# Optimization experiments

Measured on AMD Instinct MI355X. Metric: run time of the kernel, lower is better.

The kernel has to match this reference:

```python
import jax, jax.numpy as jnp
import numpy as np

RES = 32
HEADS = 16
EMB = 1024
DIM_HEAD = EMB // HEADS
BATCH = 8
N = RES * RES
SCALE = DIM_HEAD ** -0.5


def _make_bias_idxs():
    # replicate the LeViT-style |dx|,|dy| offset indexing from __init__
    points = [(i, j) for i in range(RES) for j in range(RES)]
    offsets = {}
    idxs = []
    for p1 in points:
        for p2 in points:
            off = (abs(p1[0] - p2[0]), abs(p1[1] - p2[1]))
            if off not in offsets:
                offsets[off] = len(offsets)
            idxs.append(offsets[off])
    return np.asarray(idxs, dtype=np.int32).reshape(N, N), len(offsets)


def setup_inputs() -> dict:
    key = jax.random.key(0)
    k_x, k_qkv, k_b, k_o = jax.random.split(key, 4)
    bias_idxs, n_off = _make_bias_idxs()  # n_off == 1024 for a 32x32 grid
    return {
        "x": jax.random.normal(k_x, (BATCH, N, EMB), dtype=jnp.float32),
        "W_qkv": jax.random.normal(k_qkv, (3 * EMB, EMB), dtype=jnp.float32) * 0.02,
        "attention_biases": jax.random.normal(k_b, (HEADS, n_off), dtype=jnp.float32) * 0.02,
        "bias_idxs": jnp.asarray(bias_idxs),
        "W_out": jax.random.normal(k_o, (EMB, EMB), dtype=jnp.float32) * 0.02,
        "b_out": jnp.zeros((EMB,), dtype=jnp.float32),
    }


def reference(x, W_qkv, attention_biases, bias_idxs, W_out, b_out):
    B, n, E = x.shape
    # to_qkv: Linear(E, 3E, bias=False) -> x @ W^T
    qkv = x @ W_qkv.T  # [B, n, 3E]
    q, k, v = jnp.split(qkv, 3, axis=-1)

    def heads(t):  # b n (h d) -> b h n d
        return t.reshape(B, n, HEADS, DIM_HEAD).transpose(0, 2, 1, 3)

    q, k, v = heads(q), heads(k), heads(v)
    qk = jnp.einsum("bhnd,bhmd->bhnm", q, k) * SCALE  # [B, h, n, n]
    bias = attention_biases[:, bias_idxs]  # gather -> [h, n, n]
    qk = qk + bias[None]
    attn = jax.nn.softmax(qk, axis=-1)
    out = jnp.einsum("bhnm,bhmd->bhnd", attn, v)
    out = out.transpose(0, 2, 1, 3).reshape(B, n, E)  # b h n d -> b n (h d)
    # to_out: Linear(E, E) with bias (dropout p=0 is identity)
    return out @ W_out.T + b_out
```

## Files before the change

kernel.cpp:

```cpp
#include <hip/hip_runtime.h>

typedef __attribute__((ext_vector_type(8))) short bf16x8;
typedef __attribute__((ext_vector_type(4))) short bf16x4;
typedef __attribute__((ext_vector_type(4))) float f32x4;

#define L2E 1.44269504088896340736f
#define QSCL 0.18033688011112042f

__device__ inline unsigned short f2bf(float f) {
  union { float f; unsigned int u; } x; x.f = f;
  return (unsigned short)((x.u + 0x8000u) >> 16);
}
__device__ inline unsigned int f2bf2(float a, float b) {
  union { float f; unsigned int u; } xa, xb;
  xa.f = a; xb.f = b;
  return ((xa.u + 0x8000u) >> 16) | (((xb.u + 0x8000u) & 0xFFFF0000u));
}
__device__ inline unsigned int pk_bf16(float a, float b) {
#if __has_builtin(__builtin_amdgcn_cvt_pk_bf16_f32)
  typedef __attribute__((ext_vector_type(2))) __bf16 bfv2;
  union { bfv2 v; unsigned int u; } x;
  x.v = __builtin_amdgcn_cvt_pk_bf16_f32(a, b);
  return x.u;
#else
  return f2bf2(a, b);
#endif
}

__device__ inline void gl_lds16(const void* g, void* l) {
  __builtin_amdgcn_global_load_lds((const __attribute__((address_space(1))) void*)g,
                                   (__attribute__((address_space(3))) void*)l,
                                   16, 0, 0);
}

__device__ inline void vm_drain() {
  asm volatile("s_waitcnt vmcnt(0)" ::: "memory");
}
__device__ inline void vm_wait3() {
  asm volatile("s_waitcnt vmcnt(3)" ::: "memory");
}
__device__ inline void vm_wait8() {
  asm volatile("s_waitcnt vmcnt(8)" ::: "memory");
}

__device__ inline void wave_barrier() {
  asm volatile("" ::: "memory");
  __builtin_amdgcn_s_barrier();
  asm volatile("" ::: "memory");
}

#define N4_X  2097152
#define N4_WQ 786432
#define N4_WO 262144
__global__ void cast3_kernel(const float* __restrict__ x,
                             const float* __restrict__ wq,
                             const float* __restrict__ wo,
                             unsigned short* __restrict__ xb,
                             unsigned short* __restrict__ wqb,
                             unsigned short* __restrict__ wob) {
  int i = blockIdx.x * blockDim.x + threadIdx.x;
  int st = gridDim.x * blockDim.x;
  for (; i < N4_X + N4_WQ + N4_WO; i += st) {
    const float* src; unsigned short* dst; int j;
    if (i < N4_X)            { src = x;  dst = xb;  j = i; }
    else if (i < N4_X + N4_WQ){ src = wq; dst = wqb; j = i - N4_X; }
    else                     { src = wo; dst = wob; j = i - N4_X - N4_WQ; }
    float4 v = reinterpret_cast<const float4*>(src)[j];
    ushort4 o;
    o.x = f2bf(v.x); o.y = f2bf(v.y); o.z = f2bf(v.z); o.w = f2bf(v.w);
    reinterpret_cast<ushort4*>(dst)[j] = o;
  }
}

template <int MODE>
__device__ __forceinline__ void qkv_body(
    unsigned short* lds,
    const unsigned short* __restrict__ A,
    const unsigned short* __restrict__ Bm,
    unsigned short* __restrict__ qo,
    unsigned short* __restrict__ ko,
    unsigned short* __restrict__ vo,
    int tm, int tn) {
  const int tid = threadIdx.x;
  const int w = tid >> 6, lane = tid & 63;
  const int l15 = lane & 15, quad = lane >> 4;
  const int wmb = (w >> 2) * 128;
  const int wnb = (w & 3) * 64;
  const int rl = (w << 3) + (lane >> 3);
  const int scol = ((lane & 7) ^ ((lane >> 3) & 7)) << 3;
  const int rk = l15 & 7;

  const unsigned short* Ab = A + (size_t)(tm * 256) * 1024;
  const unsigned short* Bb = Bm + (size_t)(tn * 256) * 1024;

  unsigned short* sA0 = lds;
  unsigned short* sA1 = lds + 16384;
  unsigned short* sB0 = lds + 32768;
  unsigned short* sB1 = lds + 49152;

#define STG_HALF(Gb, R0, k0, Lb)                                              \
  do {                                                                        \
    gl_lds16((Gb) + (size_t)((R0) + rl) * 1024 + (k0) + scol,                 \
             (Lb) + ((R0) + (w << 3)) * 64);                                  \
    gl_lds16((Gb) + (size_t)((R0) + 64 + rl) * 1024 + (k0) + scol,            \
             (Lb) + ((R0) + 64 + (w << 3)) * 64);                             \
  } while (0)

#define LDF(buf, row, kk) \
  (*(const bf16x8*)&(buf)[(row) * 64 + ((((kk) * 4 + quad) ^ rk) << 3)])

  STG_HALF(Ab, 0, 0, sA0);  STG_HALF(Ab, 128, 0, sA0);
  STG_HALF(Bb, 0, 0, sB0);  STG_HALF(Bb, 128, 0, sB0);
  STG_HALF(Ab, 0, 64, sA1); STG_HALF(Ab, 128, 64, sA1);
  STG_HALF(Bb, 0, 64, sB1); STG_HALF(Bb, 128, 64, sB1);

  const f32x4 fz = {0.f, 0.f, 0.f, 0.f};
  f32x4 acc[8][4];
#pragma unroll
  for (int i = 0; i < 8; i++)
#pragma unroll
    for (int j = 0; j < 4; j++) acc[i][j] = fz;

  vm_wait8();
  wave_barrier();

  for (int t = 0; t < 16; ++t) {
    unsigned short* Ac = (t & 1) ? sA1 : sA0;
    unsigned short* Bc = (t & 1) ? sB1 : sB0;
    const int kf = (t + 2) << 6;
    bf16x8 a0[4][2], a1[4][2], b0[2][2], b1[2][2];

#pragma unroll
    for (int mt = 0; mt < 4; mt++)
#pragma unroll
      for (int kk = 0; kk < 2; kk++)
        a0[mt][kk] = LDF(Ac, wmb + mt * 16 + l15, kk);
#pragma unroll
    for (int nt = 0; nt < 2; nt++)
#pragma unroll
      for (int kk = 0; kk < 2; kk++)
        b0[nt][kk] = LDF(Bc, wnb + nt * 16 + l15, kk);
    wave_barrier();
    __builtin_amdgcn_s_setprio(1);
#pragma unroll
    for (int mt = 0; mt < 4; mt++)
#pragma unroll
      for (int nt = 0; nt < 2; nt++)
#pragma unroll
        for (int kk = 0; kk < 2; kk++)
          acc[mt][nt] = (MODE == 0)
            ? __builtin_amdgcn_mfma_f32_16x16x32_bf16(b0[nt][kk], a0[mt][kk], acc[mt][nt], 0, 0, 0)
            : __builtin_amdgcn_mfma_f32_16x16x32_bf16(a0[mt][kk], b0[nt][kk], acc[mt][nt], 0, 0, 0);
    __builtin_amdgcn_s_setprio(0);
    wave_barrier();

#pragma unroll
    for (int nt = 0; nt < 2; nt++)
#pragma unroll
      for (int kk = 0; kk < 2; kk++)
        b1[nt][kk] = LDF(Bc, wnb + (nt + 2) * 16 + l15, kk);
    wave_barrier();
    __builtin_amdgcn_s_setprio(1);
#pragma unroll
    for (int mt = 0; mt < 4; mt++)
#pragma unroll
      for (int nt = 0; nt < 2; nt++)
#pragma unroll
        for (int kk = 0; kk < 2; kk++)
          acc[mt][nt + 2] = (MODE == 0)
            ? __builtin_amdgcn_mfma_f32_16x16x32_bf16(b1[nt][kk], a0[mt][kk], acc[mt][nt + 2], 0, 0, 0)
            : __builtin_amdgcn_mfma_f32_16x16x32_bf16(a0[mt][kk], b1[nt][kk], acc[mt][nt + 2], 0, 0, 0);
    __builtin_amdgcn_s_setprio(0);
    wave_barrier();

#pragma unroll
    for (int mt = 0; mt < 4; mt++)
#pragma unroll
      for (int kk = 0; kk < 2; kk++)
        a1[mt][kk] = LDF(Ac, wmb + (mt + 4) * 16 + l15, kk);
    if (t < 14) { STG_HALF(Bb, 0, kf, Bc); STG_HALF(Bb, 128, kf, Bc); }
    wave_barrier();
    __builtin_amdgcn_s_setprio(1);
#pragma unroll
    for (int mt = 0; mt < 4; mt++)
#pragma unroll
      for (int nt = 0; nt < 2; nt++)
#pragma unroll
        for (int kk = 0; kk < 2; kk++)
          acc[mt + 4][nt] = (MODE == 0)
            ? __builtin_amdgcn_mfma_f32_16x16x32_bf16(b0[nt][kk], a1[mt][kk], acc[mt + 4][nt], 0, 0, 0)
            : __builtin_amdgcn_mfma_f32_16x16x32_bf16(a1[mt][kk], b0[nt][kk], acc[mt + 4][nt], 0, 0, 0);
    __builtin_amdgcn_s_setprio(0);
    wave_barrier();

    if (t < 14) { STG_HALF(Ab, 0, kf, Ac); STG_HALF(Ab, 128, kf, Ac); }
    wave_barrier();
    __builtin_amdgcn_s_setprio(1);
#pragma unroll
    for (int mt = 0; mt < 4; mt++)
#pragma unroll
      for (int nt = 0; nt < 2; nt++)
#pragma unroll
        for (int kk = 0; kk < 2; kk++)
          acc[mt + 4][nt + 2] = (MODE == 0)
            ? __builtin_amdgcn_mfma_f32_16x16x32_bf16(b1[nt][kk], a1[mt][kk], acc[mt + 4][nt + 2], 0, 0, 0)
            : __builtin_amdgcn_mfma_f32_16x16x32_bf16(a1[mt][kk], b1[nt][kk], acc[mt + 4][nt + 2], 0, 0, 0);
    __builtin_amdgcn_s_setprio(0);
    if (t < 14) vm_wait8();
    else if (t == 14) vm_drain();
    wave_barrier();
  }
#undef STG_HALF
#undef LDF

  const int bb = tm >> 2;
  const int n0 = (tm & 3) << 8;
  const int cb = (tn & 3) << 8;
  if (MODE == 0) {
    const float scl = (tn < 4) ? QSCL : 1.0f;
    unsigned short* dst = (tn < 4) ? qo : ko;
#pragma unroll
    for (int mt = 0; mt < 8; mt++) {
      int tok = n0 + wmb + mt * 16 + l15;
#pragma unroll
      for (int nt = 0; nt < 4; nt++) {
        int c = cb + wnb + nt * 16 + quad * 4;
        int hh = c >> 6, d0 = c & 63;
        uint2 val;
        val.x = f2bf2(acc[mt][nt][0] * scl, acc[mt][nt][1] * scl);
        val.y = f2bf2(acc[mt][nt][2] * scl, acc[mt][nt][3] * scl);
        *(uint2*)&dst[(((size_t)bb * 16 + hh) * 1024 + tok) * 64 + d0] = val;
      }
    }
  } else {
#pragma unroll
    for (int mt = 0; mt < 8; mt++) {
      int tok = n0 + wmb + mt * 16 + quad * 4;
#pragma unroll
      for (int nt = 0; nt < 4; nt++) {
        int c = cb + wnb + nt * 16 + l15;
        int hh = c >> 6, dd = c & 63;
        uint2 val;
        val.x = f2bf2(acc[mt][nt][0], acc[mt][nt][1]);
        val.y = f2bf2(acc[mt][nt][2], acc[mt][nt][3]);
        *(uint2*)&vo[(((size_t)bb * 16 + hh) * 64 + dd) * 1024 + tok] = val;
      }
    }
  }
}

__global__ __launch_bounds__(512, 2) void gemm_qkv(
    const unsigned short* __restrict__ A,
    const unsigned short* __restrict__ Bm,
    unsigned short* __restrict__ qo,
    unsigned short* __restrict__ ko,
    unsigned short* __restrict__ vo) {
  __shared__ unsigned short lds[65536];
  const int id = blockIdx.x;
  const int wg = (id & 7) * 48 + (id >> 3);
  const int tm = wg / 12, tn = wg - tm * 12;
  if (tn < 8) qkv_body<0>(lds, A, Bm, qo, ko, vo, tm, tn);
  else        qkv_body<1>(lds, A, Bm, qo, ko, vo, tm, tn);
}

__global__ __launch_bounds__(256, 2) void attn_kernel(
    const unsigned short* __restrict__ Q,
    const unsigned short* __restrict__ Kg,
    const unsigned short* __restrict__ Vt,
    const float* __restrict__ biases,
    unsigned short* __restrict__ Og) {
  __shared__ unsigned short sK[2][64 * 64];
  __shared__ unsigned short sV[2][64 * 64];
  __shared__ float sBias2[32 * 63];

  const int bx = blockIdx.x;
  const int bh = bx & 127, qt = bx >> 7;
  const int h = bh & 15, b = bh >> 4;
  const int tid = threadIdx.x, w = tid >> 6, lane = tid & 63;
  const int l15 = lane & 15, quad = lane >> 4;

  const size_t bhs = (size_t)(b * 16 + h);
  const unsigned short* qbase = Q + (bhs * 1024 + (size_t)qt * 256) * 64;
  const unsigned short* kbase = Kg + bhs * 1024 * 64;
  const unsigned short* vbase = Vt + bhs * 64 * 1024;

  for (int t = tid; t < 2048; t += 256) {
    int d = t >> 6, u = t & 63;
    if (u < 63) {
      int dj = u - 31; dj = dj < 0 ? -dj : dj;
      sBias2[d * 63 + u] = biases[h * 1024 + d * 32 + dj] * L2E;
    }
  }

  const int sr0 = w * 16 + (lane >> 3);
  const int sc8 = lane & 7;
  const int sw0 = sc8 ^ (lane >> 3);

  gl_lds16(kbase + (size_t)sr0 * 64 + sw0 * 8,        &sK[0][(w * 16) * 64]);
  gl_lds16(kbase + (size_t)(sr0 + 8) * 64 + sw0 * 8,  &sK[0][(w * 16 + 8) * 64]);
  gl_lds16(vbase + (size_t)sr0 * 1024 + sw0 * 8,      &sV[0][(w * 16) * 64]);
  gl_lds16(vbase + (size_t)(sr0 + 8) * 1024 + sw0 * 8,&sV[0][(w * 16 + 8) * 64]);

  bf16x8 qf[4][2];
#pragma unroll
  for (int qb = 0; qb < 4; qb++)
#pragma unroll
    for (int kd = 0; kd < 2; kd++)
      qf[qb][kd] = *(const bf16x8*)(qbase + (w * 64 + qb * 16 + l15) * 64 + kd * 32 + quad * 8);

  const int qg0 = qt * 256 + w * 64;
  const int qtw = __builtin_amdgcn_readfirstlane(qt * 8 + w * 2);
  int cc2[2][2];
#pragma unroll
  for (int qh = 0; qh < 2; qh++)
#pragma unroll
    for (int kp = 0; kp < 2; kp++)
      cc2[qh][kp] = qh * 16 + l15 - kp * 16 - quad * 4;

  const f32x4 fz = {0.f, 0.f, 0.f, 0.f};
  f32x4 of[4][4], osum[4];
#pragma unroll
  for (int i = 0; i < 4; i++) {
    osum[i] = fz;
#pragma unroll
    for (int j = 0; j < 4; j++) of[i][j] = fz;
  }
  const bf16x4 vones = {(short)0x3F80, (short)0x3F80, (short)0x3F80, (short)0x3F80};

  int buf = 0;
  for (int j0 = 0; j0 < 1024; j0 += 64) {
    vm_drain();
    __syncthreads();
    if (j0 + 64 < 1024) {
      int nb = buf ^ 1, jn = j0 + 64;
      gl_lds16(kbase + (size_t)(jn + sr0) * 64 + sw0 * 8,       &sK[nb][(w * 16) * 64]);
      gl_lds16(kbase + (size_t)(jn + sr0 + 8) * 64 + sw0 * 8,   &sK[nb][(w * 16 + 8) * 64]);
      gl_lds16(vbase + (size_t)sr0 * 1024 + jn + sw0 * 8,       &sV[nb][(w * 16) * 64]);
      gl_lds16(vbase + (size_t)(sr0 + 8) * 1024 + jn + sw0 * 8, &sV[nb][(w * 16 + 8) * 64]);
    }
    const unsigned short* K_ = sK[buf];
    const unsigned short* V_ = sV[buf];
    const int j5 = j0 >> 5;
    const int dh = qtw - j5;
    const float* b0 = sBias2 + abs(dh) * 63 + 31;
    const float* bM = sBias2 + abs(dh - 1) * 63 + 31;
    const float* bP = sBias2 + abs(dh + 1) * 63 + 31;

#pragma unroll
    for (int kvb = 0; kvb < 4; kvb++) {
      bf16x8 kf0 = *(const bf16x8*)&K_[(kvb * 16 + l15) * 64 + ((quad ^ (l15 & 7)) << 3)];
      bf16x8 kf1 = *(const bf16x8*)&K_[(kvb * 16 + l15) * 64 + (((4 + quad) ^ (l15 & 7)) << 3)];
      bf16x4 vf[4];
#pragma unroll
      for (int nt = 0; nt < 4; nt++) {
        int d = nt * 16 + l15;
        vf[nt] = *(const bf16x4*)&V_[d * 64 + (((kvb * 2 + (quad >> 1)) ^ (l15 & 7)) << 3) + (quad & 1) * 4];
      }
      const int kp = kvb & 1;
#pragma unroll
      for (int qb = 0; qb < 4; qb++) {
        f32x4 s4 = __builtin_amdgcn_mfma_f32_16x16x32_bf16(kf0, qf[qb][0], fz, 0, 0, 0);
        s4 = __builtin_amdgcn_mfma_f32_16x16x32_bf16(kf1, qf[qb][1], s4, 0, 0, 0);
        const float* bp = (qb < 2) ? ((kvb < 2) ? b0 : bM)
                                   : ((kvb < 2) ? bP : b0);
        const float* bq = bp + cc2[qb & 1][kp];
        float p0 = __builtin_amdgcn_exp2f(s4.x + bq[0]);
        float p1 = __builtin_amdgcn_exp2f(s4.y + bq[-1]);
        float p2 = __builtin_amdgcn_exp2f(s4.z + bq[-2]);
        float p3 = __builtin_amdgcn_exp2f(s4.w + bq[-3]);
        union { unsigned int u[2]; bf16x4 v; } pk;
        pk.u[0] = pk_bf16(p0, p1);
        pk.u[1] = pk_bf16(p2, p3);
#pragma unroll
        for (int nt = 0; nt < 4; nt++)
          of[qb][nt] = __builtin_amdgcn_mfma_f32_16x16x16bf16_1k(pk.v, vf[nt], of[qb][nt], 0, 0, 0);
        osum[qb] = __builtin_amdgcn_mfma_f32_16x16x16bf16_1k(pk.v, vones, osum[qb], 0, 0, 0);
      }
    }
    buf ^= 1;
  }

  const int kvq = quad * 4;
#pragma unroll
  for (int qb = 0; qb < 4; qb++)
#pragma unroll
    for (int r = 0; r < 4; r++) {
      float inv = __builtin_amdgcn_rcpf(osum[qb][r]);
      int n = qg0 + qb * 16 + kvq + r;
      size_t orow = ((size_t)b * 1024 + n) * 1024 + h * 64;
#pragma unroll
      for (int nt = 0; nt < 4; nt++)
        Og[orow + nt * 16 + l15] = f2bf(of[qb][nt][r] * inv);
    }
}

__global__ __launch_bounds__(256, 4) void gemm_out_k(
    const unsigned short* __restrict__ A,
    const unsigned short* __restrict__ Bm,
    const float* __restrict__ bias,
    float* __restrict__ out) {
  __shared__ unsigned short sA[3][128 * 32];
  __shared__ unsigned short sB[3][64 * 32];
  const int K = 1024;
  const int tid = threadIdx.x;
  const int w = tid >> 6, lane = tid & 63;
  const int l15 = lane & 15, quad = lane >> 4;
  const int tm = blockIdx.y, tn = blockIdx.x;

  const unsigned short* Ab = A + (size_t)(tm * 128) * K;
  const unsigned short* Bb = Bm + (size_t)(tn * 64) * K;

  const int srowA = w * 32 + (lane >> 2);
  const int srowB = w * 16 + (lane >> 2);
  const int scol = (((lane & 3) ^ ((lane >> 3) & 3))) * 8;
  const int rsw = (l15 >> 1) & 3;

  const f32x4 fz = {0.f, 0.f, 0.f, 0.f};
  f32x4 acc[2][4];
#pragma unroll
  for (int i = 0; i < 2; i++)
#pragma unroll
    for (int j = 0; j < 4; j++) acc[i][j] = fz;

#define OUT_STAGE(kn, nb)                                                          \
  do {                                                                             \
    gl_lds16(Ab + (size_t)srowA * K + (kn) + scol,        &sA[nb][(w * 32) * 32]);      \
    gl_lds16(Ab + (size_t)(srowA + 16) * K + (kn) + scol, &sA[nb][(w * 32 + 16) * 32]); \
    gl_lds16(Bb + (size_t)srowB * K + (kn) + scol,        &sB[nb][(w * 16) * 32]);      \
  } while (0)

  OUT_STAGE(0, 0);
  OUT_STAGE(32, 1);

  int bi = 0;
  for (int k0 = 0; k0 < K; k0 += 32) {
    if (k0 + 64 < K) vm_wait3(); else vm_drain();
    __syncthreads();
    if (k0 + 64 < K) {
      int nb = bi + 2; if (nb >= 3) nb -= 3;
      OUT_STAGE(k0 + 64, nb);
    }
    bf16x8 af[2], bfr[4];
#pragma unroll
    for (int mt = 0; mt < 2; mt++)
      af[mt] = *(const bf16x8*)&sA[bi][(w * 32 + mt * 16 + l15) * 32 + ((quad ^ rsw) << 3)];
#pragma unroll
    for (int nt = 0; nt < 4; nt++)
      bfr[nt] = *(const bf16x8*)&sB[bi][(nt * 16 + l15) * 32 + ((quad ^ rsw) << 3)];
#pragma unroll
    for (int mt = 0; mt < 2; mt++)
#pragma unroll
      for (int nt = 0; nt < 4; nt++)
        acc[mt][nt] = __builtin_amdgcn_mfma_f32_16x16x32_bf16(af[mt], bfr[nt], acc[mt][nt], 0, 0, 0);
    bi = bi + 1; if (bi == 3) bi = 0;
  }
#undef OUT_STAGE

  const int m0 = tm * 128 + w * 32, c0 = tn * 64;
#pragma unroll
  for (int mt = 0; mt < 2; mt++)
#pragma unroll
    for (int nt = 0; nt < 4; nt++)
#pragma unroll
      for (int r = 0; r < 4; r++) {
        int m = m0 + mt * 16 + quad * 4 + r;
        int c = c0 + nt * 16 + l15;
        out[(size_t)m * 1024 + c] = acc[mt][nt][r] + bias[c];
      }
}

extern "C" void kernel_launch(void* const* d_in, const int* in_sizes, int n_in,
                              void* d_out, int out_size, void* d_ws, size_t ws_size,
                              hipStream_t stream) {
  const float* x    = (const float*)d_in[0];
  const float* Wqkv = (const float*)d_in[1];
  const float* ab   = (const float*)d_in[2];
  const float* Wout = (const float*)d_in[4];
  const float* bout = (const float*)d_in[5];
  float* out = (float*)d_out;

  char* ws = (char*)d_ws;
  unsigned short* xb  = (unsigned short*)(ws);
  unsigned short* wqb = (unsigned short*)(ws + 16777216);
  unsigned short* wob = (unsigned short*)(ws + 23068672);
  unsigned short* qw  = (unsigned short*)(ws + 25165824);
  unsigned short* kw  = (unsigned short*)(ws + 41943040);
  unsigned short* vw  = (unsigned short*)(ws + 58720256);
  unsigned short* ow  = (unsigned short*)(ws + 75497472);

  cast3_kernel<<<1536, 256, 0, stream>>>(x, Wqkv, Wout, xb, wqb, wob);
  gemm_qkv<<<384, 512, 0, stream>>>(xb, wqb, qw, kw, vw);
  attn_kernel<<<512, 256, 0, stream>>>(qw, kw, vw, ab, ow);
  gemm_out_k<<<dim3(16, 64), 256, 0, stream>>>(ow, wob, bout, out);
}
```

Before: 256.8 us.

## Restructure GEMM main loop into four M-quarter phases with next-tile fragment prefetch

```diff
diff --git a/kernel.cpp b/kernel.cpp
--- a/kernel.cpp
+++ b/kernel.cpp
@@ -38,6 +38,9 @@
 }
 __device__ inline void vm_wait3() {
   asm volatile("s_waitcnt vmcnt(3)" ::: "memory");
+}
+__device__ inline void vm_wait4() {
+  asm volatile("s_waitcnt vmcnt(4)" ::: "memory");
 }
 __device__ inline void vm_wait8() {
   asm volatile("s_waitcnt vmcnt(8)" ::: "memory");
@@ -109,6 +112,21 @@
 #define LDF(buf, row, kk) \
   (*(const bf16x8*)&(buf)[(row) * 64 + ((((kk) * 4 + quad) ^ rk) << 3)])
 
+#define MFMA_Q(q, aq)                                                          \
+  do {                                                                         \
+    _Pragma("unroll")                                                          \
+    for (int j = 0; j < 2; j++)                                                \
+      _Pragma("unroll")                                                        \
+      for (int nt = 0; nt < 4; nt++)                                           \
+        _Pragma("unroll")                                                      \
+        for (int kk = 0; kk < 2; kk++) {                                       \
+          bf16x8 bb = (nt < 2) ? bh[nt][kk] : bhi[nt - 2][kk];                 \
+          acc[2 * (q) + j][nt] = (MODE == 0)                                   \
+            ? __builtin_amdgcn_mfma_f32_16x16x32_bf16(bb, (aq)[j][kk], acc[2 * (q) + j][nt], 0, 0, 0) \
+            : __builtin_amdgcn_mfma_f32_16x16x32_bf16((aq)[j][kk], bb, acc[2 * (q) + j][nt], 0, 0, 0); \
+        }                                                                      \
+  } while (0)
+
   STG_HALF(Ab, 0, 0, sA0);  STG_HALF(Ab, 128, 0, sA0);
   STG_HALF(Bb, 0, 0, sB0);  STG_HALF(Bb, 128, 0, sB0);
   STG_HALF(Ab, 0, 64, sA1); STG_HALF(Ab, 128, 64, sA1);
@@ -124,94 +142,87 @@
   vm_wait8();
   wave_barrier();
 
+  bf16x8 ah[2][2], bh[2][2];
+#pragma unroll
+  for (int j = 0; j < 2; j++)
+#pragma unroll
+    for (int kk = 0; kk < 2; kk++) {
+      ah[j][kk] = LDF(sA0, wmb + j * 16 + l15, kk);
+      bh[j][kk] = LDF(sB0, wnb + j * 16 + l15, kk);
+    }
+
   for (int t = 0; t < 16; ++t) {
     unsigned short* Ac = (t & 1) ? sA1 : sA0;
     unsigned short* Bc = (t & 1) ? sB1 : sB0;
+    unsigned short* An = (t & 1) ? sA0 : sA1;
+    unsigned short* Bn = (t & 1) ? sB0 : sB1;
     const int kf = (t + 2) << 6;
-    bf16x8 a0[4][2], a1[4][2], b0[2][2], b1[2][2];
-
-#pragma unroll
-    for (int mt = 0; mt < 4; mt++)
+    bf16x8 a1[2][2], a2[2][2], a3[2][2], bhi[2][2], an[2][2], bn[2][2];
+
+#pragma unroll
+    for (int j = 0; j < 2; j++)
+#pragma unroll
+      for (int kk = 0; kk < 2; kk++) {
+        a1[j][kk]  = LDF(Ac, wmb + (2 + j) * 16 + l15, kk);
+        bhi[j][kk] = LDF(Bc, wnb + (2 + j) * 16 + l15, kk);
+      }
+    wave_barrier();
+    __builtin_amdgcn_s_setprio(1);
+    MFMA_Q(0, ah);
+    __builtin_amdgcn_s_setprio(0);
+    wave_barrier();
+
+#pragma unroll
+    for (int j = 0; j < 2; j++)
 #pragma unroll
       for (int kk = 0; kk < 2; kk++)
-        a0[mt][kk] = LDF(Ac, wmb + mt * 16 + l15, kk);
-#pragma unroll
-    for (int nt = 0; nt < 2; nt++)
+        a2[j][kk] = LDF(Ac, wmb + (4 + j) * 16 + l15, kk);
+    if (t < 14) { STG_HALF(Bb, 0, kf, Bc); STG_HALF(Bb, 128, kf, Bc); }
+    wave_barrier();
+    __builtin_amdgcn_s_setprio(1);
+    MFMA_Q(1, a1);
+    __builtin_amdgcn_s_setprio(0);
+    wave_barrier();
+
+#pragma unroll
+    for (int j = 0; j < 2; j++)
 #pragma unroll
       for (int kk = 0; kk < 2; kk++)
-        b0[nt][kk] = LDF(Bc, wnb + nt * 16 + l15, kk);
+        a3[j][kk] = LDF(Ac, wmb + (6 + j) * 16 + l15, kk);
     wave_barrier();
     __builtin_amdgcn_s_setprio(1);
-#pragma unroll
-    for (int mt = 0; mt < 4; mt++)
-#pragma unroll
-      for (int nt = 0; nt < 2; nt++)
-#pragma unroll
-        for (int kk = 0; kk < 2; kk++)
-          acc[mt][nt] = (MODE == 0)
-            ? __builtin_amdgcn_mfma_f32_16x16x32_bf16(b0[nt][kk], a0[mt][kk], acc[mt][nt], 0, 0, 0)
-            : __builtin_amdgcn_mfma_f32_16x16x32_bf16(a0[mt][kk], b0[nt][kk], acc[mt][nt], 0, 0, 0);
+    MFMA_Q(2, a2);
     __builtin_amdgcn_s_setprio(0);
-    wave_barrier();
-
-#pragma unroll
-    for (int nt = 0; nt < 2; nt++)
-#pragma unroll
-      for (int kk = 0; kk < 2; kk++)
-        b1[nt][kk] = LDF(Bc, wnb + (nt + 2) * 16 + l15, kk);
+    if (t < 14) vm_wait4();
+    else if (t == 14) vm_drain();
+    wave_barrier();
+
+    if (t < 15) {
+#pragma unroll
+      for (int j = 0; j < 2; j++)
+#pragma unroll
+        for (int kk = 0; kk < 2; kk++) {
+          an[j][kk] = LDF(An, wmb + j * 16 + l15, kk);
+          bn[j][kk] = LDF(Bn, wnb + j * 16 + l15, kk);
+        }
+    }
     wave_barrier();
     __builtin_amdgcn_s_setprio(1);
-#pragma unroll
-    for (int mt = 0; mt < 4; mt++)
-#pragma unroll
-      for (int nt = 0; nt < 2; nt++)
-#pragma unroll
-        for (int kk = 0; kk < 2; kk++)
-          acc[mt][nt + 2] = (MODE == 0)
-            ? __builtin_amdgcn_mfma_f32_16x16x32_bf16(b1[nt][kk], a0[mt][kk], acc[mt][nt + 2], 0, 0, 0)
-            : __builtin_amdgcn_mfma_f32_16x16x32_bf16(a0[mt][kk], b1[nt][kk], acc[mt][nt + 2], 0, 0, 0);
+    MFMA_Q(3, a3);
     __builtin_amdgcn_s_setprio(0);
-    wave_barrier();
-
-#pragma unroll
-    for (int mt = 0; mt < 4; mt++)
-#pragma unroll
-      for (int kk = 0; kk < 2; kk++)
-        a1[mt][kk] = LDF(Ac, wmb + (mt + 4) * 16 + l15, kk);
-    if (t < 14) { STG_HALF(Bb, 0, kf, Bc); STG_HALF(Bb, 128, kf, Bc); }
-    wave_barrier();
-    __builtin_amdgcn_s_setprio(1);
-#pragma unroll
-    for (int mt = 0; mt < 4; mt++)
-#pragma unroll
-      for (int nt = 0; nt < 2; nt++)
-#pragma unroll
-        for (int kk = 0; kk < 2; kk++)
-          acc[mt + 4][nt] = (MODE == 0)
-            ? __builtin_amdgcn_mfma_f32_16x16x32_bf16(b0[nt][kk], a1[mt][kk], acc[mt + 4][nt], 0, 0, 0)
-            : __builtin_amdgcn_mfma_f32_16x16x32_bf16(a1[mt][kk], b0[nt][kk], acc[mt + 4][nt], 0, 0, 0);
-    __builtin_amdgcn_s_setprio(0);
-    wave_barrier();
-
     if (t < 14) { STG_HALF(Ab, 0, kf, Ac); STG_HALF(Ab, 128, kf, Ac); }
     wave_barrier();
-    __builtin_amdgcn_s_setprio(1);
-#pragma unroll
-    for (int mt = 0; mt < 4; mt++)
-#pragma unroll
-      for (int nt = 0; nt < 2; nt++)
-#pragma unroll
-        for (int kk = 0; kk < 2; kk++)
-          acc[mt + 4][nt + 2] = (MODE == 0)
-            ? __builtin_amdgcn_mfma_f32_16x16x32_bf16(b1[nt][kk], a1[mt][kk], acc[mt + 4][nt + 2], 0, 0, 0)
-            : __builtin_amdgcn_mfma_f32_16x16x32_bf16(a1[mt][kk], b1[nt][kk], acc[mt + 4][nt + 2], 0, 0, 0);
-    __builtin_amdgcn_s_setprio(0);
-    if (t < 14) vm_wait8();
-    else if (t == 14) vm_drain();
-    wave_barrier();
+
+    if (t < 15) {
+#pragma unroll
+      for (int j = 0; j < 2; j++)
+#pragma unroll
+        for (int kk = 0; kk < 2; kk++) { ah[j][kk] = an[j][kk]; bh[j][kk] = bn[j][kk]; }
+    }
   }
 #undef STG_HALF
 #undef LDF
+#undef MFMA_Q
 
   const int bb = tm >> 2;
   const int n0 = (tm & 3) << 8;
```

Result: no change. 252.0 us (-1.9%).
